# Performance work log

Hardware: AMD Instinct MI355X
Metric: run time of the kernel (lower is better)

The kernel has to match this reference:

```python
import jax, jax.numpy as jnp
import numpy as np
import math

B, P, N, DM, H, DK, DH, DF = 2, 12, 170, 64, 8, 8, 32, 256
SQ = math.sqrt(DK)

def _ln(x, g, b):
    m = jnp.mean(x, -1, keepdims=True)
    v = jnp.var(x, -1, keepdims=True)
    return (x - m) / jnp.sqrt(v + 1e-5) * g + b

def _nozero_softmax(s):
    # faithful to nozero_softmax: mask = (s != 0), max over full row, +1e-5 in denom
    mask = (s != 0).astype(s.dtype)
    e = jnp.exp(s - jnp.max(s, -1, keepdims=True)) * mask
    return e / (jnp.sum(e, -1, keepdims=True) + 1e-5)

def _meta(c, w1, b1, w2, b2):
    # MetaLearner: [B,P,N,DM] -> [3,B,P,N,H,DK,DM]
    h = jax.nn.relu(c @ w1 + b1) @ w2 + b2
    h = h.reshape(c.shape[:3] + (3, H, DK, DM))
    return jnp.moveaxis(h, 3, 0)

def _mhlin(W, x):
    # multihead_linear_transform: per-position meta weight applied to x
    return jnp.einsum('bpnhkd,bpnd->bpnhk', W, x)

def _gdc(data, W1, W2):
    # Gated_Dynamic_Connection (noGC=False). data: [G,B,P,N,C]
    d = jnp.moveaxis(data, 0, 3)  # [B,P,N,G,C]
    a = jnp.einsum('bpngc,gcd->bpngd', d, W1)
    s = jax.nn.softmax(jax.nn.relu(jnp.einsum('bpngc,gcd->bpngd', d, W2)), axis=3)
    return jnp.sum(a * s, axis=3)  # [B,P,N,DM]

def _swish_gate(x, out, wg, bg, wo, bo):
    h = (x @ wg + bg) * out
    return (h * jax.nn.sigmoid(h)) @ wo + bo

def _spatial(Q, K, V, T):
    # adjacency-masked spatial attention. Dense-masked form is exactly the
    # scatter-into-zeros buffer of the original: zero where T==0, QK/sqrt(dk) on edges.
    s = jnp.einsum('bpihk,bpjhk->bphij', Q, K) / SQ
    Tb = T if T.ndim == 2 else T[:, :, None]  # adaptive graph [B,P,1,N,N]
    s = s * (Tb != 0)
    alpha = _nozero_softmax(s) * Tb
    return jnp.einsum('bphij,bpjhk->hbpik', alpha, V)  # [H,B,P,N,DK]

def _temporal(Q, K, V):
    s = jnp.einsum('bqnhk,bpnhk->bnhqp', Q, K) / SQ
    alpha = jax.nn.softmax(s, -1)
    return jnp.einsum('bnhqp,bpnhk->hbqnk', alpha, V)  # [H,B,P,N,DK]

def _retnet(Q, K, V, D):
    # multihead_temporal_regnet with g=1 leading dim folded in
    r = jnp.einsum('bqnhk,bpnhk->bnhqp', Q, K) / SQ
    r = r * D  # D: [H,P,P] causal decay
    rs = jnp.maximum(jnp.abs(jnp.sum(r, -1, keepdims=True)), 1.0)
    r = r / rs
    return jnp.einsum('bnhqp,bpnhk->hbqnk', r, V)  # [H,B,P,N,DK]

def _forward(x, c_x, enc, T, A, D, mr_w1, mr_b1, mr_w2, mr_b2, ms0_w1, ms0_b1, ms0_w2, ms0_b2, ms1_w1, ms1_b1, ms1_w2, ms1_b2, gr_W1, gr_W2, gs0_W1, gs0_W2, gs1_W1, gs1_W2, g2_W1, g2_W2, ge_W1, ge_W2, swr_wg, swr_bg, swr_wo, swr_bo, sws_wg, sws_bg, sws_wo, sws_bo, swe_wg, swe_bg, swe_wo, swe_bo, lnr_g, lnr_b, lns_g, lns_b, lne_g, lne_b, lnf_g, lnf_b, wq, wk, wv, f_w1, f_b1, f_w2, f_b2):
    # 1) RetNet-style temporal self retention (meta-learned QKV)
    W = _meta(c_x, mr_w1, mr_b1, mr_w2, mr_b2)
    o = _gdc(_retnet(_mhlin(W[0], x), _mhlin(W[1], x), _mhlin(W[2], x), D), gr_W1, gr_W2)
    o = _swish_gate(x, o, swr_wg, swr_bg, swr_wo, swr_bo)
    x1 = _ln(o + x, lnr_g, lnr_b)
    # 2) Spatial self attention: predefined graph + adaptive graph branches
    W0 = _meta(c_x, ms0_w1, ms0_b1, ms0_w2, ms0_b2)
    o0 = _gdc(_spatial(_mhlin(W0[0], x1), _mhlin(W0[1], x1), _mhlin(W0[2], x1), T), gs0_W1, gs0_W2)
    W1m = _meta(c_x, ms1_w1, ms1_b1, ms1_w2, ms1_b2)
    o1 = _gdc(_spatial(_mhlin(W1m[0], x1), _mhlin(W1m[1], x1), _mhlin(W1m[2], x1), A), gs1_W1, gs1_W2)
    o = _gdc(jnp.stack([o0, o1], 0), g2_W1, g2_W2)
    o = _swish_gate(x1, o, sws_wg, sws_bg, sws_wo, sws_bo)
    x2 = _ln(o + x1, lns_g, lns_b)
    # 3) Temporal encoder-decoder attention
    q = (x2 @ wq).reshape(B, P, N, H, DK)
    k = (enc @ wk).reshape(B, P, N, H, DK)
    v = (enc @ wv).reshape(B, P, N, H, DK)
    o = _gdc(_temporal(q, k, v), ge_W1, ge_W2)
    o = _swish_gate(x2, o, swe_wg, swe_bg, swe_wo, swe_bo)
    x3 = _ln(o + x2, lne_g, lne_b)
    # 4) FFN
    o = jax.nn.relu(x3 @ f_w1 + f_b1) @ f_w2 + f_b2
    return _ln(o + x3, lnf_g, lnf_b)


def setup_inputs() -> dict:
    key = jax.random.key(0)
    ks = iter(jax.random.split(key, 100))
    def rn(shape, s=0.05):
        return (jax.random.normal(next(ks), shape) * s).astype(jnp.float32)
    inp = {}
    inp['x'] = jax.random.normal(next(ks), (B, P, N, DM), jnp.float32)
    inp['c_x'] = jax.random.normal(next(ks), (B, P, N, DM), jnp.float32)
    inp['enc'] = jax.random.normal(next(ks), (B, P, N, DM), jnp.float32)
    mT = jax.random.uniform(next(ks), (N, N)) < 0.1
    inp['T'] = (jax.random.uniform(next(ks), (N, N)) * mT).astype(jnp.float32)
    mA = jax.random.uniform(next(ks), (B, P, N, N)) < 0.05
    inp['A'] = (jax.random.uniform(next(ks), (B, P, N, N)) * mA).astype(jnp.float32)
    q = np.arange(P)
    gam = 1.0 - 2.0 ** (-5.0 - np.arange(H))
    Dm = np.where(q[:, None] >= q[None, :], gam[:, None, None] ** (q[:, None] - q[None, :]), 0.0)
    inp['D'] = jnp.asarray(Dm, jnp.float32)  # [H,P,P]
    for p in ['mr', 'ms0', 'ms1']:
        inp[p + '_w1'] = rn((DM, DH)); inp[p + '_b1'] = jnp.zeros((DH,), jnp.float32)
        inp[p + '_w2'] = rn((DH, 3 * H * DK * DM)); inp[p + '_b2'] = jnp.zeros((3 * H * DK * DM,), jnp.float32)
    for p in ['gr', 'gs0', 'gs1', 'ge']:
        inp[p + '_W1'] = rn((H, DK, DM)); inp[p + '_W2'] = rn((H, DK, DM))
    inp['g2_W1'] = rn((2, DM, DM)); inp['g2_W2'] = rn((2, DM, DM))
    for p in ['swr', 'sws', 'swe']:
        inp[p + '_wg'] = rn((DM, DM)); inp[p + '_bg'] = jnp.zeros((DM,), jnp.float32)
        inp[p + '_wo'] = rn((DM, DM)); inp[p + '_bo'] = jnp.zeros((DM,), jnp.float32)
    for p in ['lnr', 'lns', 'lne', 'lnf']:
        inp[p + '_g'] = jnp.ones((DM,), jnp.float32); inp[p + '_b'] = jnp.zeros((DM,), jnp.float32)
    inp['wq'] = rn((DM, DM)); inp['wk'] = rn((DM, DM)); inp['wv'] = rn((DM, DM))
    inp['f_w1'] = rn((DM, DF)); inp['f_b1'] = jnp.zeros((DF,), jnp.float32)
    inp['f_w2'] = rn((DF, DM)); inp['f_b2'] = jnp.zeros((DM,), jnp.float32)
    return inp


def reference(x, c_x, enc, T, A, D, mr_w1, mr_b1, mr_w2, mr_b2, ms0_w1, ms0_b1, ms0_w2, ms0_b2, ms1_w1, ms1_b1, ms1_w2, ms1_b2, gr_W1, gr_W2, gs0_W1, gs0_W2, gs1_W1, gs1_W2, g2_W1, g2_W2, ge_W1, ge_W2, swr_wg, swr_bg, swr_wo, swr_bo, sws_wg, sws_bg, sws_wo, sws_bo, swe_wg, swe_bg, swe_wo, swe_bo, lnr_g, lnr_b, lns_g, lns_b, lne_g, lne_b, lnf_g, lnf_b, wq, wk, wv, f_w1, f_b1, f_w2, f_b2):
    return _forward(x, c_x, enc, T, A, D, mr_w1, mr_b1, mr_w2, mr_b2, ms0_w1, ms0_b1, ms0_w2, ms0_b2, ms1_w1, ms1_b1, ms1_w2, ms1_b2, gr_W1, gr_W2, gs0_W1, gs0_W2, gs1_W1, gs1_W2, g2_W1, g2_W2, ge_W1, ge_W2, swr_wg, swr_bg, swr_wo, swr_bo, sws_wg, sws_bg, sws_wo, sws_bo, swe_wg, swe_bg, swe_wo, swe_bo, lnr_g, lnr_b, lns_g, lns_b, lne_g, lne_b, lnf_g, lnf_b, wq, wk, wv, f_w1, f_b1, f_w2, f_b2)
```

## Files before the change

### kernel.cpp

```cpp
#include <hip/hip_runtime.h>
#include <hip/hip_bf16.h>
#include <math.h>

namespace {

constexpr int B_ = 2, P_ = 12, N_ = 170, DM_ = 64, H_ = 8, DK_ = 8, DH_ = 32, DF_ = 256;
constexpr int T_ = B_ * P_ * N_;
constexpr float SQRT_DK = 2.8284271247461903f;

constexpr int NG_ = 12;
constexpr int NC_ = 66;
constexpr int WFRAG_G = NG_ * NC_ * 64 * 8;

typedef __attribute__((ext_vector_type(4))) short short4v;
typedef __attribute__((ext_vector_type(8))) short short8v;
typedef __attribute__((ext_vector_type(4))) float float4v;

__device__ __forceinline__ unsigned short f2bf(float x) {
    union { float f; unsigned int u; } c; c.f = x;
    unsigned int r = (c.u + 0x7FFFu + ((c.u >> 16) & 1u)) >> 16;
    return (unsigned short)r;
}

__global__ void k_hr3(const float* __restrict__ c_x,
                      const float* __restrict__ w1a, const float* __restrict__ b1a,
                      const float* __restrict__ w1b, const float* __restrict__ b1b,
                      const float* __restrict__ w1c, const float* __restrict__ b1c,
                      float* __restrict__ hra, float* __restrict__ hrb,
                      float* __restrict__ hrc) {
    int z = blockIdx.y;
    const float* w1 = z == 0 ? w1a : (z == 1 ? w1b : w1c);
    const float* b1 = z == 0 ? b1a : (z == 1 ? b1b : b1c);
    float* hr = z == 0 ? hra : (z == 1 ? hrb : hrc);
    int idx = blockIdx.x * 256 + threadIdx.x;
    if (idx >= T_ * DH_) return;
    int t = idx / DH_, j = idx % DH_;
    float acc = b1[j];
    const float* cx = c_x + t * DM_;
    #pragma unroll
    for (int d = 0; d < DM_; ++d) acc += cx[d] * w1[d * DH_ + j];
    hr[idx] = fmaxf(acc, 0.f);
}

__global__ void k_wconv(const float* __restrict__ w2a, const float* __restrict__ b2a,
                        const float* __restrict__ w2b, const float* __restrict__ b2b,
                        const float* __restrict__ w2c, const float* __restrict__ b2c,
                        unsigned short* __restrict__ Wfrag) {
    int idx = blockIdx.x * 256 + threadIdx.x;
    if (idx >= 3 * NG_ * NC_ * 64) return;
    int lane = idx & 63;
    int c = (idx >> 6) % NC_;
    int ng = (idx >> 6) / NC_ % NG_;
    int g = idx / (64 * NC_ * NG_);
    const float* w2 = g == 0 ? w2a : (g == 1 ? w2b : w2c);
    const float* b2 = g == 0 ? b2a : (g == 1 ? b2b : b2c);
    int m = ng * 16 + (lane & 15);
    int u = c >> 1;
    int d0 = (c & 1) * 32 + (lane >> 4) * 8;
    const float* src = (u < DH_) ? (w2 + u * 12288 + m * 64 + d0) : (b2 + m * 64 + d0);
    short8v o;
    #pragma unroll
    for (int j = 0; j < 8; ++j) o[j] = (short)f2bf(src[j]);
    *(short8v*)(Wfrag + (size_t)idx * 8) = o;
}

__global__ __launch_bounds__(256) void k_meta_gemm2(
    const float* __restrict__ hr0, const float* __restrict__ hr1,
    const float* __restrict__ xin,
    const unsigned short* __restrict__ Wf0, const unsigned short* __restrict__ Wf1,
    float* __restrict__ out0, float* __restrict__ out1) {
    const int bz = blockIdx.z;
    const float* hr = bz ? hr1 : hr0;
    const unsigned short* Wf = bz ? Wf1 : Wf0;
    float* out = bz ? out1 : out0;

    const int tid = threadIdx.x;
    const int wv = tid >> 6, lane = tid & 63;
    const int l15 = lane & 15, quad = lane >> 4;
    const int g16 = blockIdx.x * 4 + wv;
    if (g16 >= 255) return;
    const int t = g16 * 16 + l15;
    const int nb = blockIdx.y;

    const float* xp = xin + t * 64 + quad * 8;
    float4v xa = *(const float4v*)(xp);
    float4v xb = *(const float4v*)(xp + 4);
    float4v xc = *(const float4v*)(xp + 32);
    float4v xd = *(const float4v*)(xp + 36);
    float xr[16] = {xa.x, xa.y, xa.z, xa.w, xb.x, xb.y, xb.z, xb.w,
                    xc.x, xc.y, xc.z, xc.w, xd.x, xd.y, xd.z, xd.w};

    const float* hrp = hr + t * 32;
    float4v acc[4] = {{0.f,0.f,0.f,0.f},{0.f,0.f,0.f,0.f},
                      {0.f,0.f,0.f,0.f},{0.f,0.f,0.f,0.f}};

    const unsigned short* wb = Wf + ((size_t)(nb * 4) * NC_ * 64 + lane) * 8;
    const size_t qstride = (size_t)NC_ * 64 * 8;
    const size_t cstride = 64 * 8;

    for (int u = 0; u < 33; ++u) {
        float hrv = (u < DH_) ? hrp[u] : 1.0f;
        short8v a0, a1;
        #pragma unroll
        for (int j = 0; j < 8; ++j) {
            a0[j] = (short)f2bf(hrv * xr[j]);
            a1[j] = (short)f2bf(hrv * xr[8 + j]);
        }
        const unsigned short* wc = wb + (size_t)(2 * u) * cstride;
        #pragma unroll
        for (int q = 0; q < 4; ++q) {
            short8v b0 = *(const short8v*)(wc + q * qstride);
            short8v b1 = *(const short8v*)(wc + q * qstride + cstride);
            acc[q] = __builtin_amdgcn_mfma_f32_16x16x32_bf16(a0, b0, acc[q], 0, 0, 0);
            acc[q] = __builtin_amdgcn_mfma_f32_16x16x32_bf16(a1, b1, acc[q], 0, 0, 0);
        }
    }

    #pragma unroll
    for (int q = 0; q < 4; ++q) {
        #pragma unroll
        for (int r = 0; r < 4; ++r) {
            int tt = g16 * 16 + quad * 4 + r;
            out[tt * 192 + nb * 64 + q * 16 + l15] = acc[q][r];
        }
    }
}

__global__ __launch_bounds__(256) void k_retnet(const float* __restrict__ qkv,
                                                const float* __restrict__ Dm,
                                                float* __restrict__ att) {
    const int bn = blockIdx.x;
    const int b = bn / N_, n = bn % N_;
    __shared__ float S[12][192];
    __shared__ float Ds[8 * 145];
    const int tid = threadIdx.x;
    for (int e = tid; e < 12 * 192; e += 256) {
        int p = e / 192, c = e % 192;
        S[p][c] = qkv[((size_t)((b * P_ + p) * N_ + n)) * 192 + c];
    }
    for (int e = tid; e < 1152; e += 256) {
        Ds[(e / 144) * 145 + (e % 144)] = Dm[e];
    }
    __syncthreads();
    const int qq = tid >> 6;
    const int lane = tid & 63;
    const int h = lane >> 3, k = lane & 7;
    for (int q = qq; q < P_; q += 4) {
        float Qv = S[q][h * 8 + k];
        float r[P_];
        float rsum = 0.f;
        #pragma unroll
        for (int p = 0; p < P_; ++p) {
            float prod = Qv * S[p][64 + h * 8 + k];
            prod += __shfl_xor(prod, 1, 64);
            prod += __shfl_xor(prod, 2, 64);
            prod += __shfl_xor(prod, 4, 64);
            float s = (prod / SQRT_DK) * Ds[h * 145 + q * 12 + p];
            r[p] = s; rsum += s;
        }
        float rs = fmaxf(fabsf(rsum), 1.0f);
        float acc = 0.f;
        #pragma unroll
        for (int p = 0; p < P_; ++p) acc += (r[p] / rs) * S[p][128 + h * 8 + k];
        att[((size_t)((b * P_ + q) * N_ + n)) * 64 + lane] = acc;
    }
}

__global__ __launch_bounds__(256) void k_temporal(const float* __restrict__ qkv,
                                                  float* __restrict__ att) {
    const int bn = blockIdx.x;
    const int b = bn / N_, n = bn % N_;
    __shared__ float S[12][192];
    const int tid = threadIdx.x;
    for (int e = tid; e < 12 * 192; e += 256) {
        int p = e / 192, c = e % 192;
        S[p][c] = qkv[((size_t)((b * P_ + p) * N_ + n)) * 192 + c];
    }
    __syncthreads();
    const int qq = tid >> 6;
    const int lane = tid & 63;
    const int h = lane >> 3, k = lane & 7;
    for (int q = qq; q < P_; q += 4) {
        float Qv = S[q][h * 8 + k];
        float s[P_];
        float mx = -1e30f;
        #pragma unroll
        for (int p = 0; p < P_; ++p) {
            float prod = Qv * S[p][64 + h * 8 + k];
            prod += __shfl_xor(prod, 1, 64);
            prod += __shfl_xor(prod, 2, 64);
            prod += __shfl_xor(prod, 4, 64);
            float v = prod / SQRT_DK;
            s[p] = v; mx = fmaxf(mx, v);
        }
        float den = 0.f, acc = 0.f;
        #pragma unroll
        for (int p = 0; p < P_; ++p) {
            float e = expf(s[p] - mx);
            den += e;
            acc += e * S[p][128 + h * 8 + k];
        }
        att[((size_t)((b * P_ + q) * N_ + n)) * 64 + lane] = acc / den;
    }
}

__global__ __launch_bounds__(256) void k_spatial4(
    const float* __restrict__ qkvA, const float* __restrict__ qkvB,
    const float* __restrict__ Tm, const float* __restrict__ Am,
    float* __restrict__ attA, float* __restrict__ attB) {
    const int bp = blockIdx.x;
    const int h = blockIdx.y;
    const int g = blockIdx.z >> 2;
    const int ic = blockIdx.z & 3;
    const float* qkv = g ? qkvB : qkvA;
    float* att = g ? attB : attA;

    __shared__ float sKt[8][192];
    __shared__ float sV[192][8];
    __shared__ float sW[4][192];

    const int tid = threadIdx.x;
    for (int e = tid; e < 384; e += 256) {
        int j = e >> 1, kh = (e & 1) * 4;
        float4v k4 = {0.f, 0.f, 0.f, 0.f}, v4 = k4;
        if (j < N_) {
            const float* row = qkv + (size_t)(bp * N_ + j) * 192 + h * 8 + kh;
            k4 = *(const float4v*)(row + 64);
            v4 = *(const float4v*)(row + 128);
        }
        sKt[kh + 0][j] = k4.x;
        sKt[kh + 1][j] = k4.y;
        sKt[kh + 2][j] = k4.z;
        sKt[kh + 3][j] = k4.w;
        *(float4v*)&sV[j][kh] = v4;
    }
    __syncthreads();

    const int wv = tid >> 6;
    const int lane = tid & 63;
    const int j8 = lane >> 3, kk = lane & 7;

    const int i0 = ic * 43;
    const int i1 = (i0 + 43 < N_) ? (i0 + 43) : N_;

    for (int i = i0 + wv; i < i1; i += 4) {
        const float* qrow = qkv + (size_t)(bp * N_ + i) * 192 + h * 8;
        float4v qa = *(const float4v*)qrow;
        float4v qb = *(const float4v*)(qrow + 4);
        float Qi[8] = {qa.x, qa.y, qa.z, qa.w, qb.x, qb.y, qb.z, qb.w};
        const float* Trow = g ? (Am + (size_t)(bp * N_ + i) * N_) : (Tm + (size_t)i * N_);

        float sloc[3], tloc[3];
        float mx = -1e30f;
        #pragma unroll
        for (int c = 0; c < 3; ++c) {
            int j = c * 64 + lane;
            float tv = 0.f, s = -1e30f;
            if (j < N_) {
                tv = Trow[j];
                if (tv != 0.f) {
                    float dot = 0.f;
                    #pragma unroll
                    for (int k = 0; k < 8; ++k) dot += Qi[k] * sKt[k][j];
                    s = dot / SQRT_DK;
                } else {
                    s = 0.f;
                }
            }
            sloc[c] = s; tloc[c] = tv;
            mx = fmaxf(mx, s);
        }
        #pragma unroll
        for (int off = 1; off < 64; off <<= 1) mx = fmaxf(mx, __shfl_xor(mx, off, 64));

        float den = 0.f;
        #pragma unroll
        for (int c = 0; c < 3; ++c) {
            float s = sloc[c];
            float e = (s != 0.f) ? expf(s - mx) : 0.f;
            den += e;
            sW[wv][c * 64 + lane] = e * tloc[c];
        }
        #pragma unroll
        for (int off = 1; off < 64; off <<= 1) den += __shfl_xor(den, off, 64);

        float acc = 0.f;
        #pragma unroll 4
        for (int j = j8; j < 192; j += 8) acc += sW[wv][j] * sV[j][kk];
        acc += __shfl_xor(acc, 8, 64);
        acc += __shfl_xor(acc, 16, 64);
        acc += __shfl_xor(acc, 32, 64);
        if (lane < 8)
            att[(size_t)(bp * N_ + i) * 64 + h * 8 + lane] = acc / (den + 1e-5f);
    }
}

__device__ __forceinline__ float gdc8(const float* dv, const float* W1,
                                      const float* W2, int dm) {
    float a[8], s[8];
    #pragma unroll
    for (int g = 0; g < 8; ++g) {
        float aa = 0.f, ss = 0.f;
        #pragma unroll
        for (int c = 0; c < 8; ++c) {
            float d = dv[g * 8 + c];
            aa += d * W1[(g * 8 + c) * 64 + dm];
            ss += d * W2[(g * 8 + c) * 64 + dm];
        }
        a[g] = aa; s[g] = fmaxf(ss, 0.f);
    }
    float mx = s[0];
    #pragma unroll
    for (int g = 1; g < 8; ++g) mx = fmaxf(mx, s[g]);
    float den = 0.f, o = 0.f;
    #pragma unroll
    for (int g = 0; g < 8; ++g) { float e = expf(s[g] - mx); den += e; o += a[g] * e; }
    return o / den;
}

__device__ __forceinline__ float ln_out(float r, int dm, const float* g, const float* b) {
    float m = r, m2 = r * r;
    #pragma unroll
    for (int off = 32; off; off >>= 1) { m += __shfl_xor(m, off, 64); m2 += __shfl_xor(m2, off, 64); }
    m *= (1.f / 64.f); m2 *= (1.f / 64.f);
    float var = m2 - m * m;
    return (r - m) * rsqrtf(var + 1e-5f) * g[dm] + b[dm];
}

__global__ __launch_bounds__(64) void k_gsl(const float* __restrict__ att, const float* __restrict__ xin,
    const float* W1, const float* W2,
    const float* wg, const float* bg,
    const float* wo, const float* bo,
    const float* lng, const float* lnb, float* __restrict__ xout) {
    int t = blockIdx.x, dm = threadIdx.x;
    __shared__ float dv[64], xv[64], swv[64];
    dv[dm] = att[t * 64 + dm];
    xv[dm] = xin[t * 64 + dm];
    __syncthreads();
    float o = gdc8(dv, W1, W2, dm);
    float hg = bg[dm];
    #pragma unroll
    for (int d = 0; d < 64; ++d) hg += xv[d] * wg[d * 64 + dm];
    hg *= o;
    swv[dm] = hg / (1.f + expf(-hg));
    __syncthreads();
    float ov = bo[dm];
    #pragma unroll
    for (int d = 0; d < 64; ++d) ov += swv[d] * wo[d * 64 + dm];
    float r = ov + xv[dm];
    xout[t * 64 + dm] = ln_out(r, dm, lng, lnb);
}

__global__ __launch_bounds__(64) void k_spatial_fuse(
    const float* __restrict__ att0, const float* __restrict__ att1, const float* __restrict__ x1,
    const float* gs0_W1, const float* gs0_W2,
    const float* gs1_W1, const float* gs1_W2,
    const float* g2_W1, const float* g2_W2,
    const float* wg, const float* bg,
    const float* wo, const float* bo,
    const float* lng, const float* lnb, float* __restrict__ xout) {
    int t = blockIdx.x, dm = threadIdx.x;
    __shared__ float d0[64], d1[64], o0s[64], o1s[64], xv[64], swv[64];
    d0[dm] = att0[t * 64 + dm];
    d1[dm] = att1[t * 64 + dm];
    xv[dm] = x1[t * 64 + dm];
    __syncthreads();
    o0s[dm] = gdc8(d0, gs0_W1, gs0_W2, dm);
    o1s[dm] = gdc8(d1, gs1_W1, gs1_W2, dm);
    __syncthreads();
    float a0 = 0.f, s0 = 0.f, a1 = 0.f, s1 = 0.f;
    #pragma unroll
    for (int c = 0; c < 64; ++c) {
        a0 += o0s[c] * g2_W1[c * 64 + dm];
        s0 += o0s[c] * g2_W2[c * 64 + dm];
        a1 += o1s[c] * g2_W1[(64 + c) * 64 + dm];
        s1 += o1s[c] * g2_W2[(64 + c) * 64 + dm];
    }
    s0 = fmaxf(s0, 0.f); s1 = fmaxf(s1, 0.f);
    float mx = fmaxf(s0, s1);
    float e0 = expf(s0 - mx), e1 = expf(s1 - mx);
    float o = (a0 * e0 + a1 * e1) / (e0 + e1);
    float hg = bg[dm];
    #pragma unroll
    for (int d = 0; d < 64; ++d) hg += xv[d] * wg[d * 64 + dm];
    hg *= o;
    swv[dm] = hg / (1.f + expf(-hg));
    __syncthreads();
    float ov = bo[dm];
    #pragma unroll
    for (int d = 0; d < 64; ++d) ov += swv[d] * wo[d * 64 + dm];
    float r = ov + xv[dm];
    xout[t * 64 + dm] = ln_out(r, dm, lng, lnb);
}

__global__ __launch_bounds__(64) void k_qkvproj(const float* __restrict__ x2,
    const float* __restrict__ enc,
    const float* wq, const float* wk, const float* wv,
    float* __restrict__ qkv) {
    int t = blockIdx.x, dm = threadIdx.x;
    __shared__ float xv[64], ev[64];
    xv[dm] = x2[t * 64 + dm];
    ev[dm] = enc[t * 64 + dm];
    __syncthreads();
    float aq = 0.f, ak = 0.f, av = 0.f;
    #pragma unroll
    for (int d = 0; d < 64; ++d) {
        aq += xv[d] * wq[d * 64 + dm];
        ak += ev[d] * wk[d * 64 + dm];
        av += ev[d] * wv[d * 64 + dm];
    }
    qkv[t * 192 + dm] = aq;
    qkv[t * 192 + 64 + dm] = ak;
    qkv[t * 192 + 128 + dm] = av;
}

__global__ __launch_bounds__(64) void k_ffn(const float* __restrict__ x3,
    const float* w1, const float* b1,
    const float* w2, const float* b2,
    const float* lng, const float* lnb,
    float* __restrict__ out) {
    int t = blockIdx.x, dm = threadIdx.x;
    __shared__ float xv[64], hv[256];
    xv[dm] = x3[t * 64 + dm];
    __syncthreads();
    #pragma unroll
    for (int e = 0; e < 4; ++e) {
        int j = e * 64 + dm;
        float a = b1[j];
        #pragma unroll
        for (int d = 0; d < 64; ++d) a += xv[d] * w1[d * 256 + j];
        hv[j] = fmaxf(a, 0.f);
    }
    __syncthreads();
    float a = b2[dm];
    for (int j = 0; j < 256; ++j) a += hv[j] * w2[j * 64 + dm];
    float r = a + xv[dm];
    out[t * 64 + dm] = ln_out(r, dm, lng, lnb);
}

}

extern "C" void kernel_launch(void* const* d_in, const int* in_sizes, int n_in,
                              void* d_out, int out_size, void* d_ws, size_t ws_size,
                              hipStream_t stream) {
    (void)in_sizes; (void)n_in; (void)out_size; (void)ws_size;
    const float* x    = (const float*)d_in[0];
    const float* c_x  = (const float*)d_in[1];
    const float* enc  = (const float*)d_in[2];
    const float* Tm   = (const float*)d_in[3];
    const float* Am   = (const float*)d_in[4];
    const float* Dm   = (const float*)d_in[5];
    const float* mr_w1 = (const float*)d_in[6];
    const float* mr_b1 = (const float*)d_in[7];
    const float* mr_w2 = (const float*)d_in[8];
    const float* mr_b2 = (const float*)d_in[9];
    const float* ms0_w1 = (const float*)d_in[10];
    const float* ms0_b1 = (const float*)d_in[11];
    const float* ms0_w2 = (const float*)d_in[12];
    const float* ms0_b2 = (const float*)d_in[13];
    const float* ms1_w1 = (const float*)d_in[14];
    const float* ms1_b1 = (const float*)d_in[15];
    const float* ms1_w2 = (const float*)d_in[16];
    const float* ms1_b2 = (const float*)d_in[17];
    const float* gr_W1 = (const float*)d_in[18];
    const float* gr_W2 = (const float*)d_in[19];
    const float* gs0_W1 = (const float*)d_in[20];
    const float* gs0_W2 = (const float*)d_in[21];
    const float* gs1_W1 = (const float*)d_in[22];
    const float* gs1_W2 = (const float*)d_in[23];
    const float* g2_W1 = (const float*)d_in[24];
    const float* g2_W2 = (const float*)d_in[25];
    const float* ge_W1 = (const float*)d_in[26];
    const float* ge_W2 = (const float*)d_in[27];
    const float* swr_wg = (const float*)d_in[28];
    const float* swr_bg = (const float*)d_in[29];
    const float* swr_wo = (const float*)d_in[30];
    const float* swr_bo = (const float*)d_in[31];
    const float* sws_wg = (const float*)d_in[32];
    const float* sws_bg = (const float*)d_in[33];
    const float* sws_wo = (const float*)d_in[34];
    const float* sws_bo = (const float*)d_in[35];
    const float* swe_wg = (const float*)d_in[36];
    const float* swe_bg = (const float*)d_in[37];
    const float* swe_wo = (const float*)d_in[38];
    const float* swe_bo = (const float*)d_in[39];
    const float* lnr_g = (const float*)d_in[40];
    const float* lnr_b = (const float*)d_in[41];
    const float* lns_g = (const float*)d_in[42];
    const float* lns_b = (const float*)d_in[43];
    const float* lne_g = (const float*)d_in[44];
    const float* lne_b = (const float*)d_in[45];
    const float* lnf_g = (const float*)d_in[46];
    const float* lnf_b = (const float*)d_in[47];
    const float* wq = (const float*)d_in[48];
    const float* wk = (const float*)d_in[49];
    const float* wv = (const float*)d_in[50];
    const float* f_w1 = (const float*)d_in[51];
    const float* f_b1 = (const float*)d_in[52];
    const float* f_w2 = (const float*)d_in[53];
    const float* f_b2 = (const float*)d_in[54];

    float* ws   = (float*)d_ws;
    float* hr   = ws;
    float* hr2  = hr   + T_ * DH_;
    float* qkva = hr2  + T_ * DH_;
    float* qkvb = qkva + T_ * 192;
    float* atta = qkvb + T_ * 192;
    float* attb = atta + T_ * DM_;
    float* x1f  = attb + T_ * DM_;
    float* x2f  = x1f  + T_ * DM_;
    float* x3f  = x2f  + T_ * DM_;
    unsigned short* Wfrag = (unsigned short*)(x3f + T_ * DM_);
    float* hr_r = attb;

    k_wconv<<<(3 * NG_ * NC_ * 64 + 255) / 256, 256, 0, stream>>>(
        mr_w2, mr_b2, ms0_w2, ms0_b2, ms1_w2, ms1_b2, Wfrag);

    k_hr3<<<dim3(510, 3), 256, 0, stream>>>(c_x, mr_w1, mr_b1, ms0_w1, ms0_b1,
                                            ms1_w1, ms1_b1, hr_r, hr, hr2);

    k_meta_gemm2<<<dim3(64, 3, 1), 256, 0, stream>>>(
        hr_r, hr_r, x, Wfrag, Wfrag, qkva, qkva);
    k_retnet<<<B_ * N_, 256, 0, stream>>>(qkva, Dm, atta);
    k_gsl<<<T_, 64, 0, stream>>>(atta, x, gr_W1, gr_W2, swr_wg, swr_bg, swr_wo, swr_bo,
                                 lnr_g, lnr_b, x1f);

    k_meta_gemm2<<<dim3(64, 3, 2), 256, 0, stream>>>(
        hr, hr2, x1f, Wfrag + WFRAG_G, Wfrag + 2 * WFRAG_G, qkva, qkvb);
    k_spatial4<<<dim3(B_ * P_, H_, 8), 256, 0, stream>>>(qkva, qkvb, Tm, Am, atta, attb);
    k_spatial_fuse<<<T_, 64, 0, stream>>>(atta, attb, x1f, gs0_W1, gs0_W2, gs1_W1, gs1_W2,
                                          g2_W1, g2_W2, sws_wg, sws_bg, sws_wo, sws_bo,
                                          lns_g, lns_b, x2f);

    k_qkvproj<<<T_, 64, 0, stream>>>(x2f, enc, wq, wk, wv, qkva);
    k_temporal<<<B_ * N_, 256, 0, stream>>>(qkva, atta);
    k_gsl<<<T_, 64, 0, stream>>>(atta, x2f, ge_W1, ge_W2, swe_wg, swe_bg, swe_wo, swe_bo,
                                 lne_g, lne_b, x3f);

    k_ffn<<<T_, 64, 0, stream>>>(x3f, f_w1, f_b1, f_w2, f_b2, lnf_g, lnf_b, (float*)d_out);
}
```

Before: 344.7 us.

## Batch tokens per block and stage dense weights in LDS for per-token kernels

The gated-skip, spatial-fuse, QKV-projection and FFN kernels are rewritten to process 8 or 16 tokens per 256-thread block instead of one token per 64-thread block. Each block first copies the weight matrices and biases into shared memory with vector loads, then each wave computes several tokens from LDS. The aim is to amortize the repeated global/L2 weight reads across many tokens. The cost is large LDS footprints, which lower occupancy, plus an upfront weight-load phase in every block.

```diff
diff --git a/kernel.cpp b/kernel.cpp
--- a/kernel.cpp
+++ b/kernel.cpp
@@ -327,115 +327,205 @@
     return (r - m) * rsqrtf(var + 1e-5f) * g[dm] + b[dm];
 }
 
-__global__ __launch_bounds__(64) void k_gsl(const float* __restrict__ att, const float* __restrict__ xin,
-    const float* W1, const float* W2,
-    const float* wg, const float* bg,
-    const float* wo, const float* bo,
-    const float* lng, const float* lnb, float* __restrict__ xout) {
-    int t = blockIdx.x, dm = threadIdx.x;
-    __shared__ float dv[64], xv[64], swv[64];
-    dv[dm] = att[t * 64 + dm];
-    xv[dm] = xin[t * 64 + dm];
-    __syncthreads();
-    float o = gdc8(dv, W1, W2, dm);
-    float hg = bg[dm];
-    #pragma unroll
-    for (int d = 0; d < 64; ++d) hg += xv[d] * wg[d * 64 + dm];
-    hg *= o;
-    swv[dm] = hg / (1.f + expf(-hg));
-    __syncthreads();
-    float ov = bo[dm];
-    #pragma unroll
-    for (int d = 0; d < 64; ++d) ov += swv[d] * wo[d * 64 + dm];
-    float r = ov + xv[dm];
-    xout[t * 64 + dm] = ln_out(r, dm, lng, lnb);
-}
-
-__global__ __launch_bounds__(64) void k_spatial_fuse(
-    const float* __restrict__ att0, const float* __restrict__ att1, const float* __restrict__ x1,
-    const float* gs0_W1, const float* gs0_W2,
-    const float* gs1_W1, const float* gs1_W2,
-    const float* g2_W1, const float* g2_W2,
-    const float* wg, const float* bg,
-    const float* wo, const float* bo,
-    const float* lng, const float* lnb, float* __restrict__ xout) {
-    int t = blockIdx.x, dm = threadIdx.x;
-    __shared__ float d0[64], d1[64], o0s[64], o1s[64], xv[64], swv[64];
-    d0[dm] = att0[t * 64 + dm];
-    d1[dm] = att1[t * 64 + dm];
-    xv[dm] = x1[t * 64 + dm];
-    __syncthreads();
-    o0s[dm] = gdc8(d0, gs0_W1, gs0_W2, dm);
-    o1s[dm] = gdc8(d1, gs1_W1, gs1_W2, dm);
-    __syncthreads();
-    float a0 = 0.f, s0 = 0.f, a1 = 0.f, s1 = 0.f;
-    #pragma unroll
-    for (int c = 0; c < 64; ++c) {
-        a0 += o0s[c] * g2_W1[c * 64 + dm];
-        s0 += o0s[c] * g2_W2[c * 64 + dm];
-        a1 += o1s[c] * g2_W1[(64 + c) * 64 + dm];
-        s1 += o1s[c] * g2_W2[(64 + c) * 64 + dm];
-    }
-    s0 = fmaxf(s0, 0.f); s1 = fmaxf(s1, 0.f);
-    float mx = fmaxf(s0, s1);
-    float e0 = expf(s0 - mx), e1 = expf(s1 - mx);
-    float o = (a0 * e0 + a1 * e1) / (e0 + e1);
-    float hg = bg[dm];
-    #pragma unroll
-    for (int d = 0; d < 64; ++d) hg += xv[d] * wg[d * 64 + dm];
-    hg *= o;
-    swv[dm] = hg / (1.f + expf(-hg));
-    __syncthreads();
-    float ov = bo[dm];
-    #pragma unroll
-    for (int d = 0; d < 64; ++d) ov += swv[d] * wo[d * 64 + dm];
-    float r = ov + xv[dm];
-    xout[t * 64 + dm] = ln_out(r, dm, lng, lnb);
-}
-
-__global__ __launch_bounds__(64) void k_qkvproj(const float* __restrict__ x2,
+__global__ __launch_bounds__(256) void k_gsl2(const float* __restrict__ att,
+    const float* __restrict__ xin,
+    const float* __restrict__ W1, const float* __restrict__ W2,
+    const float* __restrict__ wg, const float* __restrict__ bg,
+    const float* __restrict__ wo, const float* __restrict__ bo,
+    const float* __restrict__ lng, const float* __restrict__ lnb,
+    float* __restrict__ xout) {
+    __shared__ float W1s[4096], W2s[4096], wgs[4096], wos[4096];
+    __shared__ float bgs[64], bos[64], lngs[64], lnbs[64];
+    __shared__ float dv8[8][64], xv8[8][64], swv8[8][64];
+    const int tid = threadIdx.x;
+    const int t0 = blockIdx.x * 8;
+    for (int e = tid; e < 1024; e += 256) {
+        *(float4v*)&W1s[e * 4] = *(const float4v*)&W1[e * 4];
+        *(float4v*)&W2s[e * 4] = *(const float4v*)&W2[e * 4];
+        *(float4v*)&wgs[e * 4] = *(const float4v*)&wg[e * 4];
+        *(float4v*)&wos[e * 4] = *(const float4v*)&wo[e * 4];
+    }
+    if (tid < 64) { bgs[tid] = bg[tid]; bos[tid] = bo[tid];
+                    lngs[tid] = lng[tid]; lnbs[tid] = lnb[tid]; }
+    for (int e = tid; e < 512; e += 256) {
+        dv8[e >> 6][e & 63] = att[(size_t)(t0 + (e >> 6)) * 64 + (e & 63)];
+        xv8[e >> 6][e & 63] = xin[(size_t)(t0 + (e >> 6)) * 64 + (e & 63)];
+    }
+    __syncthreads();
+    const int wv = tid >> 6, dm = tid & 63;
+    #pragma unroll
+    for (int it = 0; it < 2; ++it) {
+        const int tt = wv + it * 4;
+        float o = gdc8(dv8[tt], W1s, W2s, dm);
+        float hg = bgs[dm];
+        #pragma unroll
+        for (int d = 0; d < 64; ++d) hg += xv8[tt][d] * wgs[d * 64 + dm];
+        hg *= o;
+        swv8[tt][dm] = hg / (1.f + expf(-hg));
+        float ov = bos[dm];
+        #pragma unroll
+        for (int d = 0; d < 64; ++d) ov += swv8[tt][d] * wos[d * 64 + dm];
+        float r = ov + xv8[tt][dm];
+        xout[(size_t)(t0 + tt) * 64 + dm] = ln_out(r, dm, lngs, lnbs);
+    }
+}
+
+__global__ __launch_bounds__(256) void k_spatial_fuse2(
+    const float* __restrict__ att0, const float* __restrict__ att1,
+    const float* __restrict__ x1,
+    const float* __restrict__ gs0_W1, const float* __restrict__ gs0_W2,
+    const float* __restrict__ gs1_W1, const float* __restrict__ gs1_W2,
+    const float* __restrict__ g2_W1, const float* __restrict__ g2_W2,
+    const float* __restrict__ wg, const float* __restrict__ bg,
+    const float* __restrict__ wo, const float* __restrict__ bo,
+    const float* __restrict__ lng, const float* __restrict__ lnb,
+    float* __restrict__ xout) {
+    __shared__ float Wbuf[24576];
+    __shared__ float d0s[16][64], d1s[16][64], x1s[16][64];
+    __shared__ float o0s[16][64], o1s[16][64], sws[16][64];
+    __shared__ float bgs[64], bos[64], lngs[64], lnbs[64];
+    const int tid = threadIdx.x;
+    const int t0 = blockIdx.x * 16;
+    for (int e = tid; e < 1024; e += 256) {
+        *(float4v*)&Wbuf[e * 4]         = *(const float4v*)&gs0_W1[e * 4];
+        *(float4v*)&Wbuf[4096 + e * 4]  = *(const float4v*)&gs0_W2[e * 4];
+        *(float4v*)&Wbuf[8192 + e * 4]  = *(const float4v*)&gs1_W1[e * 4];
+        *(float4v*)&Wbuf[12288 + e * 4] = *(const float4v*)&gs1_W2[e * 4];
+    }
+    if (tid < 64) { bgs[tid] = bg[tid]; bos[tid] = bo[tid];
+                    lngs[tid] = lng[tid]; lnbs[tid] = lnb[tid]; }
+    for (int e = tid; e < 1024; e += 256) {
+        d0s[e >> 6][e & 63] = att0[(size_t)(t0 + (e >> 6)) * 64 + (e & 63)];
+        d1s[e >> 6][e & 63] = att1[(size_t)(t0 + (e >> 6)) * 64 + (e & 63)];
+        x1s[e >> 6][e & 63] = x1[(size_t)(t0 + (e >> 6)) * 64 + (e & 63)];
+    }
+    __syncthreads();
+    const int wv = tid >> 6, dm = tid & 63;
+    #pragma unroll
+    for (int it = 0; it < 4; ++it) {
+        const int tt = wv + it * 4;
+        o0s[tt][dm] = gdc8(d0s[tt], Wbuf, Wbuf + 4096, dm);
+        o1s[tt][dm] = gdc8(d1s[tt], Wbuf + 8192, Wbuf + 12288, dm);
+    }
+    __syncthreads();
+    for (int e = tid; e < 2048; e += 256) {
+        *(float4v*)&Wbuf[e * 4]        = *(const float4v*)&g2_W1[e * 4];
+        *(float4v*)&Wbuf[8192 + e * 4] = *(const float4v*)&g2_W2[e * 4];
+    }
+    for (int e = tid; e < 1024; e += 256) {
+        *(float4v*)&Wbuf[16384 + e * 4] = *(const float4v*)&wg[e * 4];
+        *(float4v*)&Wbuf[20480 + e * 4] = *(const float4v*)&wo[e * 4];
+    }
+    __syncthreads();
+    #pragma unroll
+    for (int it = 0; it < 4; ++it) {
+        const int tt = wv + it * 4;
+        float a0 = 0.f, s0 = 0.f, a1 = 0.f, s1 = 0.f;
+        #pragma unroll
+        for (int c = 0; c < 64; ++c) {
+            float v0 = o0s[tt][c], v1 = o1s[tt][c];
+            a0 += v0 * Wbuf[c * 64 + dm];
+            s0 += v0 * Wbuf[8192 + c * 64 + dm];
+            a1 += v1 * Wbuf[4096 + c * 64 + dm];
+            s1 += v1 * Wbuf[8192 + 4096 + c * 64 + dm];
+        }
+        s0 = fmaxf(s0, 0.f); s1 = fmaxf(s1, 0.f);
+        float mx = fmaxf(s0, s1);
+        float e0 = expf(s0 - mx), e1 = expf(s1 - mx);
+        float o = (a0 * e0 + a1 * e1) / (e0 + e1);
+        float hg = bgs[dm];
+        #pragma unroll
+        for (int d = 0; d < 64; ++d) hg += x1s[tt][d] * Wbuf[16384 + d * 64 + dm];
+        hg *= o;
+        sws[tt][dm] = hg / (1.f + expf(-hg));
+        float ov = bos[dm];
+        #pragma unroll
+        for (int d = 0; d < 64; ++d) ov += sws[tt][d] * Wbuf[20480 + d * 64 + dm];
+        float r = ov + x1s[tt][dm];
+        xout[(size_t)(t0 + tt) * 64 + dm] = ln_out(r, dm, lngs, lnbs);
+    }
+}
+
+__global__ __launch_bounds__(256) void k_qkvproj2(const float* __restrict__ x2,
     const float* __restrict__ enc,
-    const float* wq, const float* wk, const float* wv,
+    const float* __restrict__ wq, const float* __restrict__ wk,
+    const float* __restrict__ wv,
     float* __restrict__ qkv) {
-    int t = blockIdx.x, dm = threadIdx.x;
-    __shared__ float xv[64], ev[64];
-    xv[dm] = x2[t * 64 + dm];
-    ev[dm] = enc[t * 64 + dm];
-    __syncthreads();
-    float aq = 0.f, ak = 0.f, av = 0.f;
-    #pragma unroll
-    for (int d = 0; d < 64; ++d) {
-        aq += xv[d] * wq[d * 64 + dm];
-        ak += ev[d] * wk[d * 64 + dm];
-        av += ev[d] * wv[d * 64 + dm];
-    }
-    qkv[t * 192 + dm] = aq;
-    qkv[t * 192 + 64 + dm] = ak;
-    qkv[t * 192 + 128 + dm] = av;
-}
-
-__global__ __launch_bounds__(64) void k_ffn(const float* __restrict__ x3,
-    const float* w1, const float* b1,
-    const float* w2, const float* b2,
-    const float* lng, const float* lnb,
+    __shared__ float wqs[4096], wks[4096], wvs[4096];
+    __shared__ float xv8[8][64], ev8[8][64];
+    const int tid = threadIdx.x;
+    const int t0 = blockIdx.x * 8;
+    for (int e = tid; e < 1024; e += 256) {
+        *(float4v*)&wqs[e * 4] = *(const float4v*)&wq[e * 4];
+        *(float4v*)&wks[e * 4] = *(const float4v*)&wk[e * 4];
+        *(float4v*)&wvs[e * 4] = *(const float4v*)&wv[e * 4];
+    }
+    for (int e = tid; e < 512; e += 256) {
+        xv8[e >> 6][e & 63] = x2[(size_t)(t0 + (e >> 6)) * 64 + (e & 63)];
+        ev8[e >> 6][e & 63] = enc[(size_t)(t0 + (e >> 6)) * 64 + (e & 63)];
+    }
+    __syncthreads();
+    const int wvx = tid >> 6, dm = tid & 63;
+    #pragma unroll
+    for (int it = 0; it < 2; ++it) {
+        const int tt = wvx + it * 4;
+        float aq = 0.f, ak = 0.f, av = 0.f;
+        #pragma unroll
+        for (int d = 0; d < 64; ++d) {
+            aq += xv8[tt][d] * wqs[d * 64 + dm];
+            ak += ev8[tt][d] * wks[d * 64 + dm];
+            av += ev8[tt][d] * wvs[d * 64 + dm];
+        }
+        const size_t t = t0 + tt;
+        qkv[t * 192 + dm] = aq;
+        qkv[t * 192 + 64 + dm] = ak;
+        qkv[t * 192 + 128 + dm] = av;
+    }
+}
+
+__global__ __launch_bounds__(256) void k_ffn2(const float* __restrict__ x3,
+    const float* __restrict__ w1, const float* __restrict__ b1,
+    const float* __restrict__ w2, const float* __restrict__ b2,
+    const float* __restrict__ lng, const float* __restrict__ lnb,
     float* __restrict__ out) {
-    int t = blockIdx.x, dm = threadIdx.x;
-    __shared__ float xv[64], hv[256];
-    xv[dm] = x3[t * 64 + dm];
-    __syncthreads();
-    #pragma unroll
-    for (int e = 0; e < 4; ++e) {
-        int j = e * 64 + dm;
-        float a = b1[j];
-        #pragma unroll
-        for (int d = 0; d < 64; ++d) a += xv[d] * w1[d * 256 + j];
-        hv[j] = fmaxf(a, 0.f);
-    }
-    __syncthreads();
-    float a = b2[dm];
-    for (int j = 0; j < 256; ++j) a += hv[j] * w2[j * 64 + dm];
-    float r = a + xv[dm];
-    out[t * 64 + dm] = ln_out(r, dm, lng, lnb);
+    __shared__ float Wbuf[16384];
+    __shared__ float hv8[8][256];
+    __shared__ float xv8[8][64];
+    __shared__ float b1s[256], b2s[64], lngs[64], lnbs[64];
+    const int tid = threadIdx.x;
+    const int t0 = blockIdx.x * 8;
+    for (int e = tid; e < 4096; e += 256)
+        *(float4v*)&Wbuf[e * 4] = *(const float4v*)&w1[e * 4];
+    if (tid < 256) b1s[tid] = b1[tid];
+    if (tid < 64) { b2s[tid] = b2[tid]; lngs[tid] = lng[tid]; lnbs[tid] = lnb[tid]; }
+    for (int e = tid; e < 512; e += 256)
+        xv8[e >> 6][e & 63] = x3[(size_t)(t0 + (e >> 6)) * 64 + (e & 63)];
+    __syncthreads();
+    const int wv = tid >> 6, dm = tid & 63;
+    #pragma unroll
+    for (int it = 0; it < 2; ++it) {
+        const int tt = wv + it * 4;
+        #pragma unroll
+        for (int e = 0; e < 4; ++e) {
+            int j = e * 64 + dm;
+            float a = b1s[j];
+            #pragma unroll
+            for (int d = 0; d < 64; ++d) a += xv8[tt][d] * Wbuf[d * 256 + j];
+            hv8[tt][j] = fmaxf(a, 0.f);
+        }
+    }
+    __syncthreads();
+    for (int e = tid; e < 4096; e += 256)
+        *(float4v*)&Wbuf[e * 4] = *(const float4v*)&w2[e * 4];
+    __syncthreads();
+    #pragma unroll
+    for (int it = 0; it < 2; ++it) {
+        const int tt = wv + it * 4;
+        float a = b2s[dm];
+        for (int j = 0; j < 256; ++j) a += hv8[tt][j] * Wbuf[j * 64 + dm];
+        float r = a + xv8[tt][dm];
+        out[(size_t)(t0 + tt) * 64 + dm] = ln_out(r, dm, lngs, lnbs);
+    }
 }
 
 }
@@ -522,20 +612,22 @@
     k_meta_gemm2<<<dim3(64, 3, 1), 256, 0, stream>>>(
         hr_r, hr_r, x, Wfrag, Wfrag, qkva, qkva);
     k_retnet<<<B_ * N_, 256, 0, stream>>>(qkva, Dm, atta);
-    k_gsl<<<T_, 64, 0, stream>>>(atta, x, gr_W1, gr_W2, swr_wg, swr_bg, swr_wo, swr_bo,
-                                 lnr_g, lnr_b, x1f);
+    k_gsl2<<<T_ / 8, 256, 0, stream>>>(atta, x, gr_W1, gr_W2, swr_wg, swr_bg,
+                                       swr_wo, swr_bo, lnr_g, lnr_b, x1f);
 
     k_meta_gemm2<<<dim3(64, 3, 2), 256, 0, stream>>>(
         hr, hr2, x1f, Wfrag + WFRAG_G, Wfrag + 2 * WFRAG_G, qkva, qkvb);
     k_spatial4<<<dim3(B_ * P_, H_, 8), 256, 0, stream>>>(qkva, qkvb, Tm, Am, atta, attb);
-    k_spatial_fuse<<<T_, 64, 0, stream>>>(atta, attb, x1f, gs0_W1, gs0_W2, gs1_W1, gs1_W2,
-                                          g2_W1, g2_W2, sws_wg, sws_bg, sws_wo, sws_bo,
-                                          lns_g, lns_b, x2f);
-
-    k_qkvproj<<<T_, 64, 0, stream>>>(x2f, enc, wq, wk, wv, qkva);
+    k_spatial_fuse2<<<T_ / 16, 256, 0, stream>>>(atta, attb, x1f,
+                                                 gs0_W1, gs0_W2, gs1_W1, gs1_W2,
+                                                 g2_W1, g2_W2, sws_wg, sws_bg,
+                                                 sws_wo, sws_bo, lns_g, lns_b, x2f);
+
+    k_qkvproj2<<<T_ / 8, 256, 0, stream>>>(x2f, enc, wq, wk, wv, qkva);
     k_temporal<<<B_ * N_, 256, 0, stream>>>(qkva, atta);
-    k_gsl<<<T_, 64, 0, stream>>>(atta, x2f, ge_W1, ge_W2, swe_wg, swe_bg, swe_wo, swe_bo,
-                                 lne_g, lne_b, x3f);
-
-    k_ffn<<<T_, 64, 0, stream>>>(x3f, f_w1, f_b1, f_w2, f_b2, lnf_g, lnf_b, (float*)d_out);
-}
+    k_gsl2<<<T_ / 8, 256, 0, stream>>>(atta, x2f, ge_W1, ge_W2, swe_wg, swe_bg,
+                                       swe_wo, swe_bo, lne_g, lne_b, x3f);
+
+    k_ffn2<<<T_ / 8, 256, 0, stream>>>(x3f, f_w1, f_b1, f_w2, f_b2, lnf_g, lnf_b,
+                                       (float*)d_out);
+}
```

Measured after the change: 517.8 us. 1.5x slower.
